# Kernel tuning notes

Hardware: AMD Instinct MI355X
Metric: run time of the kernel (lower is better)

The kernel has to match this reference:

```python
import jax, jax.numpy as jnp
import numpy as np

WH, WW = 16, 16          # window_size
C = 384                  # in_channel
H = 12                   # num_heads
HD = C // H              # head_dim = 32
B = 256                  # num_windows * batch
N = WH * WW              # tokens per window = 256
CPB_HID = 512


def _build_buffers():
    # relative_coords_table: [1, 2*WH-1, 2*WW-1, 2], log-spaced coords (pretrain_window_size = [0,0])
    rch = np.arange(-(WH - 1), WH, dtype=np.float32)
    rcw = np.arange(-(WW - 1), WW, dtype=np.float32)
    table = np.stack(np.meshgrid(rch, rcw, indexing='ij'), axis=-1)[None]  # [1,2WH-1,2WW-1,2]
    table[..., 0] /= (WH - 1)
    table[..., 1] /= (WW - 1)
    table = np.sign(table) * np.log2(np.abs(table) + 1.0) / np.log2(8)
    # relative_position_index: [N, N] int indices into flattened table
    ch = np.arange(WH)
    cw = np.arange(WW)
    coords = np.stack(np.meshgrid(ch, cw, indexing='ij'))      # [2, WH, WW]
    cf = coords.reshape(2, -1)                                  # [2, N]
    rel = cf[:, :, None] - cf[:, None, :]                       # [2, N, N]
    rel = rel.transpose(1, 2, 0).astype(np.int64)               # [N, N, 2]
    rel[..., 0] += WH - 1
    rel[..., 1] += WW - 1
    rel[..., 0] *= 2 * WW - 1
    rpi = rel.sum(-1)                                           # [N, N]
    return jnp.asarray(table, jnp.float32), jnp.asarray(rpi, jnp.int32)


def setup_inputs() -> dict:
    key = jax.random.key(0)
    ks = jax.random.split(key, 9)
    table, rpi = _build_buffers()
    return {
        'x': jax.random.normal(ks[0], (B, N, C), jnp.float32),
        'qkv_w': jax.random.normal(ks[1], (3 * C, C), jnp.float32) * 0.02,
        'q_bias': jnp.zeros((C,), jnp.float32),
        'v_bias': jnp.zeros((C,), jnp.float32),
        'logit_scale': jnp.log(10.0 * jnp.ones((H, 1, 1), jnp.float32)),
        'cpb_w1': jax.random.normal(ks[2], (CPB_HID, 2), jnp.float32) * 0.02,
        'cpb_b1': jnp.zeros((CPB_HID,), jnp.float32),
        'cpb_w2': jax.random.normal(ks[3], (H, CPB_HID), jnp.float32) * 0.02,
        'proj_w': jax.random.normal(ks[4], (C, C), jnp.float32) * 0.02,
        'proj_b': jnp.zeros((C,), jnp.float32),
        'rel_coords_table': table,
        'rel_pos_index': rpi,
    }


def reference(x, qkv_w, q_bias, v_bias, logit_scale, cpb_w1, cpb_b1, cpb_w2,
              proj_w, proj_b, rel_coords_table, rel_pos_index):
    b, n, c = x.shape
    h, hd = H, c // H
    # qkv with q/v bias, zero k bias
    bias = jnp.concatenate([q_bias, jnp.zeros_like(v_bias), v_bias])
    qkv = x @ qkv_w.T + bias                                   # [B,N,3C]
    qkv = qkv.reshape(b, n, 3, h, hd).transpose(2, 0, 3, 1, 4)  # [3,B,H,N,hd]
    q, k, v = qkv[0], qkv[1], qkv[2]
    # cosine attention: L2-normalize q, k (F.normalize with eps=1e-12)
    qn = q / jnp.maximum(jnp.linalg.norm(q, axis=-1, keepdims=True), 1e-12)
    kn = k / jnp.maximum(jnp.linalg.norm(k, axis=-1, keepdims=True), 1e-12)
    attn = jnp.einsum('bhnd,bhmd->bhnm', qn, kn)               # [B,H,N,N]
    # learnable per-head logit scale, clamped at log(1/0.01)
    scale = jnp.exp(jnp.minimum(logit_scale, jnp.log(100.0)))  # [H,1,1]
    attn = attn * scale
    # continuous relative position bias MLP: 2 -> 512 -> H
    hid = jax.nn.relu(rel_coords_table @ cpb_w1.T + cpb_b1)    # [1,2WH-1,2WW-1,512]
    bias_table = (hid @ cpb_w2.T).reshape(-1, h)               # [(2WH-1)*(2WW-1), H]
    rpb = bias_table[rel_pos_index.reshape(-1)].reshape(n, n, h).transpose(2, 0, 1)
    rpb = 16.0 * jax.nn.sigmoid(rpb)                           # [H,N,N]
    attn = jax.nn.softmax(attn + rpb, axis=-1)
    out = jnp.einsum('bhnm,bhmd->bhnd', attn, v)               # [B,H,N,hd]
    out = out.transpose(0, 2, 1, 3).reshape(b, n, c)
    return out @ proj_w.T + proj_b
```

## Files before the change

kernel.cpp:

```cpp
#include <hip/hip_runtime.h>

typedef unsigned int uint;
typedef unsigned short ushort_t;
typedef ushort_t ushort8 __attribute__((ext_vector_type(8)));
typedef ushort_t ushort4v __attribute__((ext_vector_type(4)));
typedef short short8 __attribute__((ext_vector_type(8)));
typedef float floatx4 __attribute__((ext_vector_type(4)));
typedef uint uint2v __attribute__((ext_vector_type(2)));
typedef uint uint4v __attribute__((ext_vector_type(4)));

#define WSQ 25165824L
#define NH  12
#define NT  256
#define HD  32

__device__ __forceinline__ float bf2f(ushort_t u) {
    uint x = ((uint)u) << 16;
    return __builtin_bit_cast(float, x);
}
__device__ __forceinline__ ushort_t f2bf(float f) {
    uint u = __builtin_bit_cast(uint, f);
    uint lsb = (u >> 16) & 1u;
    return (ushort_t)((u + 0x7FFFu + lsb) >> 16);
}
__device__ __forceinline__ uint cvt_pk_bf16(float lo, float hi) {
    uint r;
    asm("v_cvt_pk_bf16_f32 %0, %1, %2" : "=v"(r) : "v"(lo), "v"(hi));
    return r;
}
__device__ __forceinline__ float exp2_fast(float x) {
    float r;
    asm("v_exp_f32 %0, %1" : "=v"(r) : "v"(x));
    return r;
}
__device__ __forceinline__ float ld1(const void* p, long i, int f) {
    return f ? ((const float*)p)[i] : bf2f(((const ushort_t*)p)[i]);
}

__global__ void detect_kernel(const ushort_t* __restrict__ x, int* __restrict__ flag) {
    int t = threadIdx.x;
    uint u = x[2 * t];
    int e = (u >> 7) & 0xFF;
    int weird = (e > 147 || e < 107) ? 1 : 0;
    unsigned long long b = __ballot(weird);
    if (t == 0) *flag = (__popcll(b) > 19) ? 1 : 0;
}

__global__ __launch_bounds__(256) void cvt_kernel(
    const void* __restrict__ src, ushort_t* __restrict__ dst,
    const int* __restrict__ fl, long n8)
{
    long i = (long)blockIdx.x * 256 + threadIdx.x;
    if (i >= n8) return;
    if (*fl) {
        const floatx4* s = (const floatx4*)((const float*)src + i * 8);
        floatx4 a = s[0], b = s[1];
        ushort8 o;
        for (int j = 0; j < 4; ++j) { o[j] = f2bf(a[j]); o[4 + j] = f2bf(b[j]); }
        *(ushort8*)(dst + i * 8) = o;
    } else {
        *(ushort8*)(dst + i * 8) = *(const ushort8*)((const ushort_t*)src + i * 8);
    }
}

__global__ __launch_bounds__(512) void cpb_kernel(
    const void* __restrict__ tab, const void* __restrict__ w1,
    const void* __restrict__ b1, const void* __restrict__ w2,
    const int* __restrict__ fl, float* __restrict__ bt)
{
    __shared__ float hid[512];
    const int f = *fl;
    int p = blockIdx.x, j = threadIdx.x;
    float c0 = ld1(tab, p * 2 + 0, f);
    float c1 = ld1(tab, p * 2 + 1, f);
    float v = ld1(w1, j * 2 + 0, f) * c0 + ld1(w1, j * 2 + 1, f) * c1 + ld1(b1, j, f);
    hid[j] = fmaxf(v, 0.0f);
    __syncthreads();
    if (j < NH) {
        float s = 0.0f;
        for (int i = 0; i < 512; ++i) s += hid[i] * ld1(w2, (long)j * 512 + i, f);
        bt[p * NH + j] = s;
    }
}

__global__ __launch_bounds__(256) void rpb_kernel(
    const int* __restrict__ rpi, const float* __restrict__ bt,
    float* __restrict__ rpb)
{
    int idx = blockIdx.x * 256 + threadIdx.x;
    int h = idx >> 16, ij = idx & 65535;
    float x = bt[rpi[ij] * NH + h];
    rpb[idx] = 1.44269504f * 16.0f / (1.0f + __expf(-x));
}

template <int MODE>
__global__ __launch_bounds__(256) void gemm_bt(
    const ushort_t* __restrict__ A, const ushort_t* __restrict__ Bw,
    const void* __restrict__ bias0, const void* __restrict__ bias2,
    void* __restrict__ Cout, const int* __restrict__ fl)
{
    const int K = 384;
    __shared__ ushort_t As[128 * 72];
    __shared__ ushort_t Bs[128 * 72];
    const int f = *fl;
    const int tid = threadIdx.x;
    const int w = tid >> 6, lane = tid & 63, l15 = lane & 15, quad = lane >> 4;
    const int m0 = blockIdx.y * 128, n0 = blockIdx.x * 128;
    const int rw = (w >> 1) * 64, cw = (w & 1) * 64;
    const int lr = tid >> 3, lc = (tid & 7) * 8;

    floatx4 acc[4][4] = {};
    ushort8 pa[4], pb[4];

    for (int i = 0; i < 4; ++i) {
        int r = lr + i * 32;
        if (MODE == 0) {
            pa[i] = *(const ushort8*)&A[(long)(m0 + r) * K + lc];
        } else {
            int m = m0 + r, kc = lc;
            long ad = ((long)(m >> 8) * 12 + (kc >> 5)) * 8192 + (m & 255) * 32 + (kc & 31);
            pa[i] = *(const ushort8*)&A[ad];
        }
        pb[i] = *(const ushort8*)&Bw[(long)(n0 + r) * K + lc];
    }

    for (int kt = 0; kt < K; kt += 64) {
        for (int i = 0; i < 4; ++i) {
            int r = lr + i * 32;
            *(ushort8*)&As[r * 72 + lc] = pa[i];
            *(ushort8*)&Bs[r * 72 + lc] = pb[i];
        }
        __syncthreads();
        if (kt + 64 < K) {
            for (int i = 0; i < 4; ++i) {
                int r = lr + i * 32;
                if (MODE == 0) {
                    pa[i] = *(const ushort8*)&A[(long)(m0 + r) * K + kt + 64 + lc];
                } else {
                    int m = m0 + r, kc = kt + 64 + lc;
                    long ad = ((long)(m >> 8) * 12 + (kc >> 5)) * 8192 + (m & 255) * 32 + (kc & 31);
                    pa[i] = *(const ushort8*)&A[ad];
                }
                pb[i] = *(const ushort8*)&Bw[(long)(n0 + r) * K + kt + 64 + lc];
            }
        }
        for (int ks = 0; ks < 64; ks += 32) {
            short8 af[4], bfr[4];
            for (int mt = 0; mt < 4; ++mt)
                af[mt] = *(short8*)&As[(rw + mt * 16 + l15) * 72 + ks + quad * 8];
            for (int nt = 0; nt < 4; ++nt)
                bfr[nt] = *(short8*)&Bs[(cw + nt * 16 + l15) * 72 + ks + quad * 8];
            for (int mt = 0; mt < 4; ++mt)
                for (int nt = 0; nt < 4; ++nt)
                    acc[mt][nt] = __builtin_amdgcn_mfma_f32_16x16x32_bf16(
                        af[mt], bfr[nt], acc[mt][nt], 0, 0, 0);
        }
        __syncthreads();
    }

    for (int mt = 0; mt < 4; ++mt) {
        for (int nt = 0; nt < 4; ++nt) {
            int c = n0 + cw + nt * 16 + l15;
            if (MODE == 0) {
                int which = c / 384, cc = c % 384;
                float bias = (which == 0) ? ld1(bias0, cc, f)
                           : (which == 2) ? ld1(bias2, cc, f) : 0.0f;
                int hh = cc >> 5, dd = cc & 31;
                for (int r = 0; r < 4; ++r) {
                    int m = m0 + rw + mt * 16 + quad * 4 + r;
                    int b = m >> 8, ntok = m & 255;
                    long dst = (long)which * WSQ +
                               (((long)(b * NH + hh) * NT + ntok) * HD + dd);
                    ((ushort_t*)Cout)[dst] = f2bf(acc[mt][nt][r] + bias);
                }
            } else {
                float bias = ld1(bias0, c, f);
                for (int r = 0; r < 4; ++r) {
                    int m = m0 + rw + mt * 16 + quad * 4 + r;
                    float v = acc[mt][nt][r] + bias;
                    long o = (long)m * 384 + c;
                    if (f) ((float*)Cout)[o] = v;
                    else   ((ushort_t*)Cout)[o] = f2bf(v);
                }
            }
        }
    }
}

__global__ __launch_bounds__(128) void attn_kernel(
    ushort_t* __restrict__ qkv, const void* __restrict__ ls,
    const float* __restrict__ rpb, const int* __restrict__ fl)
{
    __shared__ __attribute__((aligned(16))) ushort_t ks[256 * 40];
    __shared__ __attribute__((aligned(16))) ushort_t vts[32 * 264];
    __shared__ __attribute__((aligned(16))) ushort_t ps[2 * 16 * 40];

    const int f = *fl;
    const int bh = blockIdx.x;
    const int b = bh / NH, h = bh % NH;
    ushort_t* qp = qkv + (long)bh * NT * HD;
    const ushort_t* kp = qp + WSQ;
    const ushort_t* vp = qp + 2 * WSQ;
    const int tid = threadIdx.x;
    const float scale = __expf(fminf(ld1(ls, h, f), 4.6051702f)) * 1.44269504f;

    for (int t = tid; t < 256; t += 128) {
        ushort8 kv[4];
        #pragma unroll
        for (int i = 0; i < 4; ++i) kv[i] = *(const ushort8*)&kp[t * HD + i * 8];
        float fv[32]; float ss = 0.0f;
        #pragma unroll
        for (int i = 0; i < 4; ++i)
            #pragma unroll
            for (int j = 0; j < 8; ++j) {
                float v = bf2f(kv[i][j]); fv[i * 8 + j] = v; ss += v * v;
            }
        float rn = 1.0f / fmaxf(sqrtf(ss), 1e-12f);
        #pragma unroll
        for (int i = 0; i < 4; ++i) {
            uint4v o;
            #pragma unroll
            for (int j = 0; j < 4; ++j)
                o[j] = cvt_pk_bf16(fv[i * 8 + 2 * j] * rn, fv[i * 8 + 2 * j + 1] * rn);
            *(uint4v*)&ks[t * 40 + i * 8] = o;
        }
        ushort8 vv[4];
        #pragma unroll
        for (int i = 0; i < 4; ++i) vv[i] = *(const ushort8*)&vp[t * HD + i * 8];
        #pragma unroll
        for (int i = 0; i < 4; ++i)
            #pragma unroll
            for (int j = 0; j < 8; ++j) vts[(i * 8 + j) * 264 + t] = vv[i][j];
    }
    __syncthreads();

    const int w = tid >> 6, lane = tid & 63, l15 = lane & 15, quad = lane >> 4;
    ushort_t* psw = &ps[w * 16 * 40];

    for (int c = 0; c < 8; ++c) {
        const int mloc = w * 128 + c * 16;

        ushort8 qv = *(const ushort8*)&qp[(mloc + l15) * HD + quad * 8];
        float qf[8]; float ss = 0.0f;
        #pragma unroll
        for (int j = 0; j < 8; ++j) { qf[j] = bf2f(qv[j]); ss += qf[j] * qf[j]; }
        ss += __shfl_xor(ss, 16, 64);
        ss += __shfl_xor(ss, 32, 64);
        float rn = 1.0f / fmaxf(sqrtf(ss), 1e-12f);
        uint4v qa;
        #pragma unroll
        for (int j = 0; j < 4; ++j)
            qa[j] = cvt_pk_bf16(qf[2 * j] * rn, qf[2 * j + 1] * rn);
        short8 aq = __builtin_bit_cast(short8, qa);

        floatx4 accS[16];
        #pragma unroll
        for (int t = 0; t < 16; ++t) {
            short8 bk = *(short8*)&ks[(t * 16 + l15) * 40 + quad * 8];
            floatx4 z = {};
            accS[t] = __builtin_amdgcn_mfma_f32_16x16x32_bf16(bk, aq, z, 0, 0, 0);
        }

        const float* rp = rpb + ((long)h * NT + mloc + l15) * NT;
        float m4[4] = {-3e38f, -3e38f, -3e38f, -3e38f};
        #pragma unroll
        for (int t = 0; t < 16; ++t) {
            floatx4 rb = *(const floatx4*)&rp[t * 16 + quad * 4];
            float v0 = fmaf(accS[t][0], scale, rb[0]);
            float v1 = fmaf(accS[t][1], scale, rb[1]);
            float v2 = fmaf(accS[t][2], scale, rb[2]);
            float v3 = fmaf(accS[t][3], scale, rb[3]);
            accS[t][0] = v0; accS[t][1] = v1; accS[t][2] = v2; accS[t][3] = v3;
            m4[t & 3] = fmaxf(m4[t & 3], fmaxf(fmaxf(v0, v1), fmaxf(v2, v3)));
        }
        float rmax = fmaxf(fmaxf(m4[0], m4[1]), fmaxf(m4[2], m4[3]));
        rmax = fmaxf(rmax, __shfl_xor(rmax, 16, 64));
        rmax = fmaxf(rmax, __shfl_xor(rmax, 32, 64));

        float s4[4] = {0.f, 0.f, 0.f, 0.f};
        floatx4 accO[2] = {};
        #pragma unroll
        for (int kk = 0; kk < 8; ++kk) {
            #pragma unroll
            for (int th = 0; th < 2; ++th) {
                int t = kk * 2 + th;
                float p0 = exp2_fast(accS[t][0] - rmax);
                float p1 = exp2_fast(accS[t][1] - rmax);
                float p2 = exp2_fast(accS[t][2] - rmax);
                float p3 = exp2_fast(accS[t][3] - rmax);
                s4[0] += p0; s4[1] += p1; s4[2] += p2; s4[3] += p3;
                uint2v po;
                po[0] = cvt_pk_bf16(p0, p1);
                po[1] = cvt_pk_bf16(p2, p3);
                *(uint2v*)&psw[l15 * 40 + th * 16 + quad * 4] = po;
            }
            short8 pf = *(short8*)&psw[l15 * 40 + quad * 8];
            #pragma unroll
            for (int tn = 0; tn < 2; ++tn) {
                short8 vf = *(short8*)&vts[(tn * 16 + l15) * 264 + kk * 32 + quad * 8];
                accO[tn] = __builtin_amdgcn_mfma_f32_16x16x32_bf16(pf, vf, accO[tn], 0, 0, 0);
            }
        }

        float rsum = (s4[0] + s4[1]) + (s4[2] + s4[3]);
        rsum += __shfl_xor(rsum, 16, 64);
        rsum += __shfl_xor(rsum, 32, 64);
        float rinv = 1.0f / rsum;
        float ri[4];
        #pragma unroll
        for (int r = 0; r < 4; ++r) ri[r] = __shfl(rinv, quad * 4 + r, 64);

        #pragma unroll
        for (int tn = 0; tn < 2; ++tn)
            #pragma unroll
            for (int r = 0; r < 4; r += 2) {
                uint pk = cvt_pk_bf16(accO[tn][r] * ri[r], accO[tn][r + 1] * ri[r + 1]);
                int n = mloc + quad * 4 + r;
                qp[n * HD + tn * 16 + l15] = (ushort_t)pk;
                qp[(n + 1) * HD + tn * 16 + l15] = (ushort_t)(pk >> 16);
            }
    }
}

extern "C" void kernel_launch(void* const* d_in, const int* in_sizes, int n_in,
                              void* d_out, int out_size, void* d_ws, size_t ws_size,
                              hipStream_t stream)
{
    const void* x      = d_in[0];
    const void* qkv_w  = d_in[1];
    const void* q_bias = d_in[2];
    const void* v_bias = d_in[3];
    const void* lscale = d_in[4];
    const void* cpb_w1 = d_in[5];
    const void* cpb_b1 = d_in[6];
    const void* cpb_w2 = d_in[7];
    const void* proj_w = d_in[8];
    const void* proj_b = d_in[9];
    const void* rct    = d_in[10];
    const int*  rpi    = (const int*)d_in[11];

    char* ws = (char*)d_ws;
    ushort_t* qkv_ws  = (ushort_t*)ws;
    float*    bt      = (float*)(ws + 150994944L);
    float*    rpb     = (float*)(ws + 151060480L);
    int*      flag    = (int*)(ws + 154206208L);
    ushort_t* wqkv_b  = (ushort_t*)(ws + 154206464L);
    ushort_t* wproj_b = (ushort_t*)(ws + 155091200L);
    ushort_t* xb      = (ushort_t*)d_out;

    detect_kernel<<<1, 64, 0, stream>>>((const ushort_t*)x, flag);
    cvt_kernel<<<12288, 256, 0, stream>>>(x, xb, flag, 3145728L);
    cvt_kernel<<<216, 256, 0, stream>>>(qkv_w, wqkv_b, flag, 55296L);
    cvt_kernel<<<72, 256, 0, stream>>>(proj_w, wproj_b, flag, 18432L);
    cpb_kernel<<<961, 512, 0, stream>>>(rct, cpb_w1, cpb_b1, cpb_w2, flag, bt);
    rpb_kernel<<<3072, 256, 0, stream>>>(rpi, bt, rpb);
    gemm_bt<0><<<dim3(9, 512), 256, 0, stream>>>(xb, wqkv_b, q_bias, v_bias, qkv_ws, flag);
    attn_kernel<<<3072, 128, 0, stream>>>(qkv_ws, lscale, rpb, flag);
    gemm_bt<1><<<dim3(3, 512), 256, 0, stream>>>(qkv_ws, wproj_b, proj_b, nullptr, d_out, flag);
}
```

Measured before the change: 510.9 us.

## Use permlane swaps for P fragment, widen attention blocks to 4 waves

The softmax probabilities are now rearranged from the QK MFMA output layout into the PV MFMA A-operand layout with permlane32/permlane16 swaps in registers. This replaces the round trip through a per-wave LDS staging buffer. The attention kernel also moves from 2 to 4 waves per block, so each wave handles 64 query rows instead of 128 and the K/V staging is done one row per thread. The aim is to cut LDS traffic and waits in the inner loop and to raise parallelism per block, at the cost of register pressure under the launch_bounds(256,4) constraint.

```diff
diff --git a/kernel.cpp b/kernel.cpp
--- a/kernel.cpp
+++ b/kernel.cpp
@@ -32,6 +32,14 @@
     float r;
     asm("v_exp_f32 %0, %1" : "=v"(r) : "v"(x));
     return r;
+}
+__device__ __forceinline__ void permlane32_swap(uint& a, uint& b) {
+    uint2v r = __builtin_amdgcn_permlane32_swap(a, b, false, false);
+    a = r[0]; b = r[1];
+}
+__device__ __forceinline__ void permlane16_swap(uint& a, uint& b) {
+    uint2v r = __builtin_amdgcn_permlane16_swap(a, b, false, false);
+    a = r[0]; b = r[1];
 }
 __device__ __forceinline__ float ld1(const void* p, long i, int f) {
     return f ? ((const float*)p)[i] : bf2f(((const ushort_t*)p)[i]);
@@ -187,24 +195,24 @@
     }
 }
 
-__global__ __launch_bounds__(128) void attn_kernel(
+__global__ __launch_bounds__(256, 4) void attn_kernel(
     ushort_t* __restrict__ qkv, const void* __restrict__ ls,
     const float* __restrict__ rpb, const int* __restrict__ fl)
 {
     __shared__ __attribute__((aligned(16))) ushort_t ks[256 * 40];
     __shared__ __attribute__((aligned(16))) ushort_t vts[32 * 264];
-    __shared__ __attribute__((aligned(16))) ushort_t ps[2 * 16 * 40];
 
     const int f = *fl;
     const int bh = blockIdx.x;
-    const int b = bh / NH, h = bh % NH;
+    const int h = bh % NH;
     ushort_t* qp = qkv + (long)bh * NT * HD;
     const ushort_t* kp = qp + WSQ;
     const ushort_t* vp = qp + 2 * WSQ;
     const int tid = threadIdx.x;
     const float scale = __expf(fminf(ld1(ls, h, f), 4.6051702f)) * 1.44269504f;
 
-    for (int t = tid; t < 256; t += 128) {
+    {
+        const int t = tid;
         ushort8 kv[4];
         #pragma unroll
         for (int i = 0; i < 4; ++i) kv[i] = *(const ushort8*)&kp[t * HD + i * 8];
@@ -235,10 +243,9 @@
     __syncthreads();
 
     const int w = tid >> 6, lane = tid & 63, l15 = lane & 15, quad = lane >> 4;
-    ushort_t* psw = &ps[w * 16 * 40];
-
-    for (int c = 0; c < 8; ++c) {
-        const int mloc = w * 128 + c * 16;
+
+    for (int c = 0; c < 4; ++c) {
+        const int mloc = w * 64 + c * 16;
 
         ushort8 qv = *(const ushort8*)&qp[(mloc + l15) * HD + quad * 8];
         float qf[8]; float ss = 0.0f;
@@ -281,25 +288,27 @@
         floatx4 accO[2] = {};
         #pragma unroll
         for (int kk = 0; kk < 8; ++kk) {
-            #pragma unroll
-            for (int th = 0; th < 2; ++th) {
-                int t = kk * 2 + th;
-                float p0 = exp2_fast(accS[t][0] - rmax);
-                float p1 = exp2_fast(accS[t][1] - rmax);
-                float p2 = exp2_fast(accS[t][2] - rmax);
-                float p3 = exp2_fast(accS[t][3] - rmax);
-                s4[0] += p0; s4[1] += p1; s4[2] += p2; s4[3] += p3;
-                uint2v po;
-                po[0] = cvt_pk_bf16(p0, p1);
-                po[1] = cvt_pk_bf16(p2, p3);
-                *(uint2v*)&psw[l15 * 40 + th * 16 + quad * 4] = po;
-            }
-            short8 pf = *(short8*)&psw[l15 * 40 + quad * 8];
-            #pragma unroll
-            for (int tn = 0; tn < 2; ++tn) {
-                short8 vf = *(short8*)&vts[(tn * 16 + l15) * 264 + kk * 32 + quad * 8];
-                accO[tn] = __builtin_amdgcn_mfma_f32_16x16x32_bf16(pf, vf, accO[tn], 0, 0, 0);
-            }
+            short8 vf0 = *(short8*)&vts[l15 * 264 + kk * 32 + quad * 8];
+            short8 vf1 = *(short8*)&vts[(16 + l15) * 264 + kk * 32 + quad * 8];
+            const int t0 = 2 * kk, t1 = 2 * kk + 1;
+            float a0 = exp2_fast(accS[t0][0] - rmax);
+            float a1 = exp2_fast(accS[t0][1] - rmax);
+            float a2 = exp2_fast(accS[t0][2] - rmax);
+            float a3 = exp2_fast(accS[t0][3] - rmax);
+            float b0 = exp2_fast(accS[t1][0] - rmax);
+            float b1 = exp2_fast(accS[t1][1] - rmax);
+            float b2 = exp2_fast(accS[t1][2] - rmax);
+            float b3 = exp2_fast(accS[t1][3] - rmax);
+            s4[0] += a0 + b0; s4[1] += a1 + b1;
+            s4[2] += a2 + b2; s4[3] += a3 + b3;
+            uint A0 = cvt_pk_bf16(a0, a1), A1 = cvt_pk_bf16(a2, a3);
+            uint B0 = cvt_pk_bf16(b0, b1), B1 = cvt_pk_bf16(b2, b3);
+            permlane32_swap(A0, B0); permlane16_swap(A0, B0);
+            permlane32_swap(A1, B1); permlane16_swap(A1, B1);
+            uint4v pw; pw[0] = A0; pw[1] = A1; pw[2] = B0; pw[3] = B1;
+            short8 pf = __builtin_bit_cast(short8, pw);
+            accO[0] = __builtin_amdgcn_mfma_f32_16x16x32_bf16(pf, vf0, accO[0], 0, 0, 0);
+            accO[1] = __builtin_amdgcn_mfma_f32_16x16x32_bf16(pf, vf1, accO[1], 0, 0, 0);
         }
 
         float rsum = (s4[0] + s4[1]) + (s4[2] + s4[3]);
@@ -355,6 +364,6 @@
     cpb_kernel<<<961, 512, 0, stream>>>(rct, cpb_w1, cpb_b1, cpb_w2, flag, bt);
     rpb_kernel<<<3072, 256, 0, stream>>>(rpi, bt, rpb);
     gemm_bt<0><<<dim3(9, 512), 256, 0, stream>>>(xb, wqkv_b, q_bias, v_bias, qkv_ws, flag);
-    attn_kernel<<<3072, 128, 0, stream>>>(qkv_ws, lscale, rpb, flag);
+    attn_kernel<<<3072, 256, 0, stream>>>(qkv_ws, lscale, rpb, flag);
     gemm_bt<1><<<dim3(3, 512), 256, 0, stream>>>(qkv_ws, wproj_b, proj_b, nullptr, d_out, flag);
 }
```

After: 502.8 us. Within noise of the previous version (-1.6%).
